# Kernel optimization log

Measured on AMD Instinct MI355X. Metric: run time of the kernel, lower is better.

Reference implementation:

```python
import jax, jax.numpy as jnp
import numpy as np
from jax import lax

DIM, DH, HEADS, IMG, P = 3, 32, 8, 64, 16
INNER = DH * HEADS            # 256
PATCH_DIM = DIM * P * P       # 768
HP = IMG // P                 # 4
EPS = 1e-5


def _conv3(x, w):
    # 3x3, stride 1, pad 1, no bias (NCHW / OIHW)
    return lax.conv_general_dilated(x, w, (1, 1), ((1, 1), (1, 1)),
                                    dimension_numbers=('NCHW', 'OIHW', 'NCHW'))


def _ln(x, g, b):
    mu = jnp.mean(x, axis=-1, keepdims=True)
    var = jnp.mean(jnp.square(x - mu), axis=-1, keepdims=True)
    return (x - mu) * lax.rsqrt(var + EPS) * g + b


def _attn(q, k, v):
    # q,k,v: [b, h, n, d]
    scores = jnp.einsum('bhnd,bhmd->bhnm', q, k) / np.float32(np.sqrt(DH))
    w = jax.nn.softmax(scores, axis=-1)
    return jnp.einsum('bhnm,bhmd->bhnd', w, v)


def _split_heads(qkv, b, n):
    # qkv: [b, n, 3*INNER] -> three [b, heads, n, dh]
    q, k, v = jnp.split(qkv, 3, axis=-1)
    f = lambda t: t.reshape(b, n, HEADS, DH).transpose(0, 2, 1, 3)
    return f(q), f(k), f(v)


def setup_inputs() -> dict:
    key = jax.random.key(0)
    ks = jax.random.split(key, 16)
    s = 0.02
    inp = {
        'x': jax.random.normal(ks[0], (1, DIM, IMG, IMG), jnp.float32),
        'pe_w1': jax.random.normal(ks[1], (DIM, DIM, 3, 3), jnp.float32) * s,
        'pe_w2': jax.random.normal(ks[2], (DIM, DIM, 3, 3), jnp.float32) * s,
        'embed_w': jax.random.normal(ks[3], (PATCH_DIM, DIM, P, P), jnp.float32) * s,
        'embed_b': jnp.zeros((PATCH_DIM,), jnp.float32),
        'ln1_g': jnp.ones((PATCH_DIM,), jnp.float32),
        'ln1_b': jnp.zeros((PATCH_DIM,), jnp.float32),
        'qkv_patch_w': jax.random.normal(ks[4], (PATCH_DIM, 3 * INNER), jnp.float32) * s,
        'proj_patch_w': jax.random.normal(ks[5], (INNER, PATCH_DIM), jnp.float32) * s,
        'proj_patch_b': jnp.zeros((PATCH_DIM,), jnp.float32),
        'recon_w': jax.random.normal(ks[6], (PATCH_DIM, DIM, P, P), jnp.float32) * s,
        'recon_b': jnp.zeros((DIM,), jnp.float32),
        'ln2_g': jnp.ones((DIM,), jnp.float32),
        'ln2_b': jnp.zeros((DIM,), jnp.float32),
        'qkv_seq_w': jax.random.normal(ks[7], (DIM, 3 * INNER), jnp.float32) * s,
        'proj_seq_w': jax.random.normal(ks[8], (INNER, DIM), jnp.float32) * s,
        'proj_seq_b': jnp.zeros((DIM,), jnp.float32),
        'pd_w1': jax.random.normal(ks[9], (DIM, DIM, 3, 3), jnp.float32) * s,
        'pd_w2': jax.random.normal(ks[10], (DIM, DIM, 3, 3), jnp.float32) * s,
    }
    return inp


def reference(x, pe_w1, pe_w2, embed_w, embed_b, ln1_g, ln1_b, qkv_patch_w,
              proj_patch_w, proj_patch_b, recon_w, recon_b, ln2_g, ln2_b,
              qkv_seq_w, proj_seq_w, proj_seq_b, pd_w1, pd_w2):
    b, c, h, w = x.shape
    pos = _conv3(jax.nn.gelu(_conv3(x, pe_w1), approximate=False), pe_w2)

    # ---- patch branch: strided conv == patch einsum ----
    xp = pos.reshape(b, c, HP, P, HP, P)
    patches = jnp.einsum('bchpwq,ocpq->bohw', xp, embed_w) + embed_b[None, :, None, None]
    patches = patches.reshape(b, PATCH_DIM, HP * HP).transpose(0, 2, 1)  # [b, 16, 768]
    pn = _ln(patches, ln1_g, ln1_b)
    q, k, v = _split_heads(pn @ qkv_patch_w, b, HP * HP)
    op = _attn(q, k, v)                                       # [b, heads, 16, dh]
    op = op.transpose(0, 2, 1, 3).reshape(b, HP * HP, INNER)
    op = op @ proj_patch_w + proj_patch_b                     # [b, 16, 768]
    op = op.transpose(0, 2, 1).reshape(b, PATCH_DIM, HP, HP)
    # ConvTranspose2d with k = stride = P -> einsum + reshape
    out_patch = jnp.einsum('bchw,cdij->bdhiwj', op, recon_w).reshape(b, DIM, h, w)
    out_patch = out_patch + recon_b[None, :, None, None]

    # ---- pixel-level branch: full dense attention over N = h*w tokens ----
    seq = pos.reshape(b, c, h * w).transpose(0, 2, 1)          # [b, N, 3]
    sn = _ln(seq, ln2_g, ln2_b)
    qs, ks_, vs = _split_heads(sn @ qkv_seq_w, b, h * w)
    os_ = _attn(qs, ks_, vs)                                   # [b, heads, N, dh]
    os_ = os_.transpose(0, 2, 1, 3).reshape(b, h * w, INNER)
    os_ = os_ @ proj_seq_w + proj_seq_b                         # [b, N, 3]
    out_seq = os_.transpose(0, 2, 1).reshape(b, DIM, h, w)

    combined = out_patch + out_seq
    return _conv3(jax.nn.gelu(_conv3(combined, pd_w1), approximate=False), pd_w2)
```

## Files before the change

### kernel.cpp

```cpp
#include <hip/hip_runtime.h>
#include <math.h>

#define NPIX 4096

__device__ __forceinline__ float gelu_exact(float x) {
    return 0.5f * x * (1.0f + erff(x * 0.70710678118654752440f));
}

__device__ __forceinline__ float conv3_tap(const float* __restrict__ src,
                                           const float* __restrict__ w,
                                           int o, int y, int x) {
    float acc = 0.f;
#pragma unroll
    for (int ci = 0; ci < 3; ++ci) {
#pragma unroll
        for (int dy = 0; dy < 3; ++dy) {
            int yy = y + dy - 1;
            if (yy < 0 || yy >= 64) continue;
#pragma unroll
            for (int dx = 0; dx < 3; ++dx) {
                int xx = x + dx - 1;
                if (xx < 0 || xx >= 64) continue;
                acc = fmaf(src[ci*NPIX + yy*64 + xx], w[o*27 + ci*9 + dy*3 + dx], acc);
            }
        }
    }
    return acc;
}

__global__ void kA(const float* __restrict__ x, const float* __restrict__ pew1,
                   const float* __restrict__ qsw, const float* __restrict__ psw,
                   float* __restrict__ t1, float* __restrict__ MT) {
    int b = blockIdx.x, tid = threadIdx.x;
    if (b < 48) {
        int idx = b*256 + tid;
        int c = idx >> 12, rem = idx & 4095;
        t1[idx] = gelu_exact(conv3_tap(x, pew1, c, rem >> 6, rem & 63));
    } else if (tid < 144) {
        int isT = tid >= 72;
        int u = isT ? tid - 72 : tid;
        int h = u / 9, i = (u % 9) / 3, j = u % 3;
        float acc = 0.f;
        if (!isT) {
            const float* wq = qsw + i*768 + h*32;
            const float* wk = qsw + j*768 + 256 + h*32;
#pragma unroll
            for (int d = 0; d < 32; ++d) acc = fmaf(wq[d], wk[d], acc);
            acc *= 1.4426950408889634f * 0.17677669529663687f;
        } else {
            const float* wv = qsw + i*768 + 512 + h*32;
#pragma unroll
            for (int d = 0; d < 32; ++d) acc = fmaf(wv[d], psw[(h*32 + d)*3 + j], acc);
        }
        MT[tid] = acc;
    }
}

__global__ void kB(const float* __restrict__ t1, const float* __restrict__ pew2,
                   const float* __restrict__ lg, const float* __restrict__ lb,
                   float* __restrict__ pos, float* __restrict__ sn,
                   float* __restrict__ z1, float* __restrict__ z2,
                   float* __restrict__ z3, float* __restrict__ z4) {
    int n = blockIdx.x*256 + threadIdx.x;
    int y = n >> 6, x = n & 63;
    float p0 = conv3_tap(t1, pew2, 0, y, x);
    float p1 = conv3_tap(t1, pew2, 1, y, x);
    float p2 = conv3_tap(t1, pew2, 2, y, x);
    float mu = (p0 + p1 + p2) * (1.f/3.f);
    float d0 = p0 - mu, d1 = p1 - mu, d2 = p2 - mu;
    float r = rsqrtf((d0*d0 + d1*d1 + d2*d2) * (1.f/3.f) + 1e-5f);
    pos[n] = p0; pos[NPIX+n] = p1; pos[2*NPIX+n] = p2;
    sn[n]        = d0*r*lg[0] + lb[0];
    sn[NPIX+n]   = d1*r*lg[1] + lb[1];
    sn[2*NPIX+n] = d2*r*lg[2] + lb[2];
#pragma unroll
    for (int i = 0; i < 3; ++i) {
        z1[i*NPIX+n] = 0.f; z2[i*NPIX+n] = 0.f;
        z3[i*NPIX+n] = 0.f; z4[i*NPIX+n] = 0.f;
    }
}

__global__ void kC1(const float* __restrict__ pos, const float* __restrict__ ew,
                    float* __restrict__ pb) {
    __shared__ float pv[16*96];
    int och = blockIdx.x % 3, ks = blockIdx.x / 3;
    int k0 = ks * 96, tid = threadIdx.x;
    for (int idx = tid; idx < 1536; idx += 256) {
        int t = idx / 96, k = idx % 96;
        int kk = k0 + k;
        int c = kk >> 8, p = (kk >> 4) & 15, q = kk & 15;
        int hp = t >> 2, wp = t & 3;
        pv[idx] = pos[c*NPIX + (hp*16 + p)*64 + wp*16 + q];
    }
    __syncthreads();
    int o = och*256 + tid;
    float acc[16];
#pragma unroll
    for (int t = 0; t < 16; ++t) acc[t] = 0.f;
    const float4* wr = (const float4*)(ew + o*768 + k0);
#pragma unroll 2
    for (int k4 = 0; k4 < 24; ++k4) {
        float4 w4 = wr[k4];
#pragma unroll
        for (int t = 0; t < 16; ++t) {
            const float* p4 = &pv[t*96 + k4*4];
            acc[t] = fmaf(w4.x, p4[0], acc[t]);
            acc[t] = fmaf(w4.y, p4[1], acc[t]);
            acc[t] = fmaf(w4.z, p4[2], acc[t]);
            acc[t] = fmaf(w4.w, p4[3], acc[t]);
        }
    }
#pragma unroll
    for (int t = 0; t < 16; ++t) atomicAdd(&pb[t*768 + o], acc[t]);
}

__global__ void kC2(const float* __restrict__ pb, const float* __restrict__ eb,
                    const float* __restrict__ g, const float* __restrict__ bb,
                    float* __restrict__ pn) {
    __shared__ float rs[12], rs2[12], stats[2];
    int t = blockIdx.x, tid = threadIdx.x;
    float v = pb[t*768 + tid] + eb[tid];
    float s = v, s2 = v*v;
#pragma unroll
    for (int o = 32; o >= 1; o >>= 1) { s += __shfl_xor(s, o); s2 += __shfl_xor(s2, o); }
    int wid = tid >> 6;
    if ((tid & 63) == 0) { rs[wid] = s; rs2[wid] = s2; }
    __syncthreads();
    if (tid == 0) {
        float S = 0.f, S2 = 0.f;
        for (int i = 0; i < 12; ++i) { S += rs[i]; S2 += rs2[i]; }
        float mu = S * (1.f/768.f);
        stats[0] = mu;
        stats[1] = rsqrtf(fmaxf(S2 * (1.f/768.f) - mu*mu, 0.f) + 1e-5f);
    }
    __syncthreads();
    pn[t*768 + tid] = (v - stats[0]) * stats[1] * g[tid] + bb[tid];
}

__global__ void kD(const float* __restrict__ pn, const float* __restrict__ qw,
                   float* __restrict__ qkvp) {
    __shared__ float ps[16*48];
    int och = blockIdx.x % 3, ks = blockIdx.x / 3;
    int k0 = ks * 48, tid = threadIdx.x;
    for (int idx = tid; idx < 768; idx += 256) {
        int t = idx / 48, k = idx % 48;
        ps[idx] = pn[t*768 + k0 + k];
    }
    __syncthreads();
    int o = och*256 + tid;
    float acc[16];
#pragma unroll
    for (int t = 0; t < 16; ++t) acc[t] = 0.f;
    for (int k = 0; k < 48; ++k) {
        float w = qw[(k0 + k)*768 + o];
#pragma unroll
        for (int t = 0; t < 16; ++t) acc[t] = fmaf(ps[t*48 + k], w, acc[t]);
    }
#pragma unroll
    for (int t = 0; t < 16; ++t) atomicAdd(&qkvp[t*768 + o], acc[t]);
}

__global__ __launch_bounds__(512) void kE(const float* __restrict__ qkvp,
                                          float* __restrict__ attn) {
    __shared__ float qs[16*772];
    __shared__ float wsm[8][16][16];
    int tid = threadIdx.x;
    for (int i = tid; i < 3072; i += 512) {
        int n = i / 192, c4 = i % 192;
        ((float4*)&qs[n*772])[c4] = ((const float4*)qkvp)[i];
    }
    __syncthreads();
    int h = tid >> 6, l = tid & 63;
    int nn = l >> 2, mg = l & 3;
    const float* q = &qs[nn*772 + h*32];
    float sc[4];
#pragma unroll
    for (int mm = 0; mm < 4; ++mm) {
        int m = mg*4 + mm;
        const float* k = &qs[m*772 + 256 + h*32];
        float d = 0.f;
#pragma unroll
        for (int dd = 0; dd < 32; ++dd) d = fmaf(q[dd], k[dd], d);
        sc[mm] = d * 0.17677669529663687f;
    }
    float mx = fmaxf(fmaxf(sc[0], sc[1]), fmaxf(sc[2], sc[3]));
    mx = fmaxf(mx, __shfl_xor(mx, 1));
    mx = fmaxf(mx, __shfl_xor(mx, 2));
    float e[4]; float sum = 0.f;
#pragma unroll
    for (int mm = 0; mm < 4; ++mm) { e[mm] = expf(sc[mm] - mx); sum += e[mm]; }
    sum += __shfl_xor(sum, 1);
    sum += __shfl_xor(sum, 2);
    float inv = 1.f / sum;
#pragma unroll
    for (int mm = 0; mm < 4; ++mm) wsm[h][nn][mg*4 + mm] = e[mm] * inv;
    __syncthreads();
    int flat = tid * 8;
    int h2 = flat >> 9, n2 = (flat >> 5) & 15, d0 = flat & 31;
    float out[8];
#pragma unroll
    for (int r = 0; r < 8; ++r) out[r] = 0.f;
#pragma unroll
    for (int m = 0; m < 16; ++m) {
        float ww = wsm[h2][n2][m];
        const float* v = &qs[m*772 + 512 + h2*32 + d0];
#pragma unroll
        for (int r = 0; r < 8; ++r) out[r] = fmaf(ww, v[r], out[r]);
    }
#pragma unroll
    for (int r = 0; r < 8; ++r) attn[n2*256 + h2*32 + d0 + r] = out[r];
}

__global__ void kF1(const float* __restrict__ at, const float* __restrict__ pw,
                    float* __restrict__ op) {
    __shared__ float as_[16*64];
    int och = blockIdx.x % 3, ks = blockIdx.x / 3;
    int k0 = ks * 64, tid = threadIdx.x;
    for (int idx = tid; idx < 1024; idx += 256) {
        int t = idx >> 6, k = idx & 63;
        as_[idx] = at[t*256 + k0 + k];
    }
    __syncthreads();
    int o = och*256 + tid;
    float acc[16];
#pragma unroll
    for (int t = 0; t < 16; ++t) acc[t] = 0.f;
    for (int k = 0; k < 64; ++k) {
        float w = pw[(k0 + k)*768 + o];
#pragma unroll
        for (int t = 0; t < 16; ++t) acc[t] = fmaf(as_[t*64 + k], w, acc[t]);
    }
#pragma unroll
    for (int t = 0; t < 16; ++t) atomicAdd(&op[t*768 + o], acc[t]);
}

__global__ void kF2(const float* __restrict__ op, const float* __restrict__ ppb,
                    const float* __restrict__ rw, float* __restrict__ outp) {
    __shared__ float os_[16*96];
    int dch = blockIdx.x % 3, cs = blockIdx.x / 3;
    int c0 = cs * 96, tid = threadIdx.x;
    for (int idx = tid; idx < 1536; idx += 256) {
        int t = idx / 96, k = idx % 96;
        os_[idx] = op[t*768 + c0 + k] + ppb[c0 + k];
    }
    __syncthreads();
    int dij = dch*256 + tid;
    float acc[16];
#pragma unroll
    for (int t = 0; t < 16; ++t) acc[t] = 0.f;
    for (int k = 0; k < 96; ++k) {
        float w = rw[(c0 + k)*768 + dij];
#pragma unroll
        for (int t = 0; t < 16; ++t) acc[t] = fmaf(os_[t*96 + k], w, acc[t]);
    }
    int d = dij >> 8, i = (dij >> 4) & 15, j = dij & 15;
#pragma unroll
    for (int t = 0; t < 16; ++t) {
        int hp = t >> 2, wp = t & 3;
        atomicAdd(&outp[d*NPIX + (hp*16 + i)*64 + wp*16 + j], acc[t]);
    }
}

__global__ __launch_bounds__(256) void kG(const float* __restrict__ snG,
                                          const float* __restrict__ MT,
                                          const float* __restrict__ psb,
                                          float* __restrict__ outs) {
    __shared__ float s[12288];
    __shared__ float Msh[72], Tsh[72];
    __shared__ float acc[8][3];
    int tid = threadIdx.x;
    for (int i = tid; i < 3072; i += 256)
        ((float4*)s)[i] = ((const float4*)snG)[i];
    if (tid < 72) Msh[tid] = MT[tid];
    else if (tid < 144) Tsh[tid - 72] = MT[tid];
    if (tid < 24) acc[tid / 3][tid % 3] = 0.f;
    __syncthreads();

    int pair = tid >> 2, chunk = tid & 3;
    int h = pair & 7, nl = pair >> 3;
    int n = blockIdx.x*8 + nl;
    float x0 = s[n], x1 = s[4096 + n], x2 = s[8192 + n];
    const float* M = &Msh[h*9];
    float a0 = x0*M[0] + x1*M[3] + x2*M[6];
    float a1 = x0*M[1] + x1*M[4] + x2*M[7];
    float a2 = x0*M[2] + x1*M[5] + x2*M[8];
    float Z = 0.f, S0 = 0.f, S1 = 0.f, S2 = 0.f;
#pragma unroll 4
    for (int t4 = 0; t4 < 1024; ++t4) {
        int m = t4*4 + chunk;
        float v0 = s[m], v1 = s[4096 + m], v2 = s[8192 + m];
        float e = exp2f(fmaf(a0, v0, fmaf(a1, v1, a2 * v2)));
        Z += e;
        S0 = fmaf(e, v0, S0); S1 = fmaf(e, v1, S1); S2 = fmaf(e, v2, S2);
    }
#pragma unroll
    for (int o = 1; o <= 2; o <<= 1) {
        Z  += __shfl_xor(Z, o);  S0 += __shfl_xor(S0, o);
        S1 += __shfl_xor(S1, o); S2 += __shfl_xor(S2, o);
    }
    if (chunk == 0) {
        float inv = 1.f / Z;
        float r0 = S0*inv, r1 = S1*inv, r2 = S2*inv;
        const float* T = &Tsh[h*9];
        atomicAdd(&acc[nl][0], r0*T[0] + r1*T[3] + r2*T[6]);
        atomicAdd(&acc[nl][1], r0*T[1] + r1*T[4] + r2*T[7]);
        atomicAdd(&acc[nl][2], r0*T[2] + r1*T[5] + r2*T[8]);
    }
    __syncthreads();
    if (tid < 24) {
        int j = tid % 3, nn = tid / 3;
        outs[j*NPIX + blockIdx.x*8 + nn] = acc[nn][j] + psb[j];
    }
}

__global__ void kH(const float* __restrict__ outp, const float* __restrict__ outs,
                   const float* __restrict__ rb, const float* __restrict__ w,
                   float* __restrict__ t2) {
    int idx = blockIdx.x*256 + threadIdx.x;
    int c = idx >> 12, rem = idx & 4095;
    int y = rem >> 6, x = rem & 63;
    float acc = 0.f;
#pragma unroll
    for (int ci = 0; ci < 3; ++ci) {
        float bias = rb[ci];
#pragma unroll
        for (int dy = 0; dy < 3; ++dy) {
            int yy = y + dy - 1;
            if (yy < 0 || yy >= 64) continue;
#pragma unroll
            for (int dx = 0; dx < 3; ++dx) {
                int xx = x + dx - 1;
                if (xx < 0 || xx >= 64) continue;
                float cb = outp[ci*NPIX + yy*64 + xx] + bias + outs[ci*NPIX + yy*64 + xx];
                acc = fmaf(cb, w[c*27 + ci*9 + dy*3 + dx], acc);
            }
        }
    }
    t2[idx] = gelu_exact(acc);
}

__global__ void kI(const float* __restrict__ t2, const float* __restrict__ w,
                   float* __restrict__ out) {
    int idx = blockIdx.x*256 + threadIdx.x;
    int c = idx >> 12, rem = idx & 4095;
    out[idx] = conv3_tap(t2, w, c, rem >> 6, rem & 63);
}

extern "C" void kernel_launch(void* const* d_in, const int* in_sizes, int n_in,
                              void* d_out, int out_size, void* d_ws, size_t ws_size,
                              hipStream_t stream) {
    (void)in_sizes; (void)n_in; (void)out_size; (void)ws_size;
    const float* x    = (const float*)d_in[0];
    const float* pew1 = (const float*)d_in[1];
    const float* pew2 = (const float*)d_in[2];
    const float* ew   = (const float*)d_in[3];
    const float* eb   = (const float*)d_in[4];
    const float* g1   = (const float*)d_in[5];
    const float* b1   = (const float*)d_in[6];
    const float* qpw  = (const float*)d_in[7];
    const float* ppw  = (const float*)d_in[8];
    const float* ppb  = (const float*)d_in[9];
    const float* rw   = (const float*)d_in[10];
    const float* rb   = (const float*)d_in[11];
    const float* g2   = (const float*)d_in[12];
    const float* b2   = (const float*)d_in[13];
    const float* qsw  = (const float*)d_in[14];
    const float* psw  = (const float*)d_in[15];
    const float* psb  = (const float*)d_in[16];
    const float* pdw1 = (const float*)d_in[17];
    const float* pdw2 = (const float*)d_in[18];

    float* ws   = (float*)d_ws;
    float* t1   = ws;
    float* pos  = ws + 12288;
    float* sn   = ws + 24576;
    float* MT   = ws + 36864;
    float* pb   = ws + 37008;
    float* pn   = ws + 49296;
    float* qkvp = ws + 61584;
    float* attn = ws + 73872;
    float* op   = ws + 77968;
    float* outp = ws + 90256;
    float* outs = ws + 102544;
    float* t2   = ws + 114832;
    float* out  = (float*)d_out;

    kA<<<dim3(49),  dim3(256), 0, stream>>>(x, pew1, qsw, psw, t1, MT);
    kB<<<dim3(16),  dim3(256), 0, stream>>>(t1, pew2, g2, b2, pos, sn, pb, qkvp, op, outp);
    kC1<<<dim3(24), dim3(256), 0, stream>>>(pos, ew, pb);
    kC2<<<dim3(16), dim3(768), 0, stream>>>(pb, eb, g1, b1, pn);
    kD<<<dim3(48),  dim3(256), 0, stream>>>(pn, qpw, qkvp);
    kE<<<dim3(1),   dim3(512), 0, stream>>>(qkvp, attn);
    kF1<<<dim3(12), dim3(256), 0, stream>>>(attn, ppw, op);
    kF2<<<dim3(24), dim3(256), 0, stream>>>(op, ppb, rw, outp);
    kG<<<dim3(512), dim3(256), 0, stream>>>(sn, MT, psb, outs);
    kH<<<dim3(48),  dim3(256), 0, stream>>>(outp, outs, rb, pdw1, t2);
    kI<<<dim3(48),  dim3(256), 0, stream>>>(t2, pdw2, out);
}
```

Measured before the change: 244.3 us.

## Fuse conv stages, merge pixel attention with embed GEMM, restructure patch attention

Merges the first two 3x3 convs into one kernel with a halo-recomputed intermediate in shared memory, and does the same for the final two convs. The pixel-attention kernel is rewritten so each thread handles one key subset for all eight heads using a hardware exp2. That kernel also shares a launch with the patch-embedding GEMM, which now uses a finer K split. Patch attention is folded into the output-projection kernel, and the kD and kF2 K-splits are doubled. The aim is to cut launch count, global round-trips and serial tail kernels, at the cost of redundant halo recomputation and more atomics.

```diff
diff --git a/kernel.cpp b/kernel.cpp
--- a/kernel.cpp
+++ b/kernel.cpp
@@ -2,6 +2,12 @@
 #include <math.h>
 
 #define NPIX 4096
+
+#if __has_builtin(__builtin_amdgcn_exp2f)
+#define EXP2(x) __builtin_amdgcn_exp2f(x)
+#else
+#define EXP2(x) exp2f(x)
+#endif
 
 __device__ __forceinline__ float gelu_exact(float x) {
     return 0.5f * x * (1.0f + erff(x * 0.70710678118654752440f));
@@ -28,90 +34,199 @@
     return acc;
 }
 
-__global__ void kA(const float* __restrict__ x, const float* __restrict__ pew1,
-                   const float* __restrict__ qsw, const float* __restrict__ psw,
-                   float* __restrict__ t1, float* __restrict__ MT) {
+__global__ __launch_bounds__(256) void kAB(
+        const float* __restrict__ x, const float* __restrict__ pew1,
+        const float* __restrict__ pew2,
+        const float* __restrict__ lg, const float* __restrict__ lb,
+        const float* __restrict__ qsw, const float* __restrict__ psw,
+        float* __restrict__ pos, float* __restrict__ sn, float* __restrict__ MT,
+        float* __restrict__ z1, float* __restrict__ z2,
+        float* __restrict__ z3, float* __restrict__ z4) {
     int b = blockIdx.x, tid = threadIdx.x;
-    if (b < 48) {
-        int idx = b*256 + tid;
-        int c = idx >> 12, rem = idx & 4095;
-        t1[idx] = gelu_exact(conv3_tap(x, pew1, c, rem >> 6, rem & 63));
-    } else if (tid < 144) {
-        int isT = tid >= 72;
-        int u = isT ? tid - 72 : tid;
-        int h = u / 9, i = (u % 9) / 3, j = u % 3;
+    if (b == 16) {
+        if (tid < 144) {
+            int isT = tid >= 72;
+            int u = isT ? tid - 72 : tid;
+            int h = u / 9, i = (u % 9) / 3, j = u % 3;
+            float acc = 0.f;
+            if (!isT) {
+                const float* wq = qsw + i*768 + h*32;
+                const float* wk = qsw + j*768 + 256 + h*32;
+#pragma unroll
+                for (int d = 0; d < 32; ++d) acc = fmaf(wq[d], wk[d], acc);
+                acc *= 1.4426950408889634f * 0.17677669529663687f;
+            } else {
+                const float* wv = qsw + i*768 + 512 + h*32;
+#pragma unroll
+                for (int d = 0; d < 32; ++d) acc = fmaf(wv[d], psw[(h*32 + d)*3 + j], acc);
+            }
+            MT[tid] = acc;
+        }
+        return;
+    }
+    __shared__ float t1l[3][8][64];
+    int y0 = b * 4;
+    for (int i = tid; i < 1536; i += 256) {
+        int c = i >> 9, rr = (i >> 6) & 7, xx = i & 63;
+        int yg = y0 - 2 + rr;
+        float v = 0.f;
+        if (yg >= 0 && yg < 64) v = gelu_exact(conv3_tap(x, pew1, c, yg, xx));
+        t1l[c][rr][xx] = v;
+    }
+    __syncthreads();
+    int n = b*256 + tid;
+    int yl = tid >> 6;
+    int xx = tid & 63;
+    int yg = y0 + yl;
+    float p[3];
+#pragma unroll
+    for (int o = 0; o < 3; ++o) {
         float acc = 0.f;
-        if (!isT) {
-            const float* wq = qsw + i*768 + h*32;
-            const float* wk = qsw + j*768 + 256 + h*32;
-#pragma unroll
-            for (int d = 0; d < 32; ++d) acc = fmaf(wq[d], wk[d], acc);
-            acc *= 1.4426950408889634f * 0.17677669529663687f;
-        } else {
-            const float* wv = qsw + i*768 + 512 + h*32;
-#pragma unroll
-            for (int d = 0; d < 32; ++d) acc = fmaf(wv[d], psw[(h*32 + d)*3 + j], acc);
-        }
-        MT[tid] = acc;
-    }
-}
-
-__global__ void kB(const float* __restrict__ t1, const float* __restrict__ pew2,
-                   const float* __restrict__ lg, const float* __restrict__ lb,
-                   float* __restrict__ pos, float* __restrict__ sn,
-                   float* __restrict__ z1, float* __restrict__ z2,
-                   float* __restrict__ z3, float* __restrict__ z4) {
-    int n = blockIdx.x*256 + threadIdx.x;
-    int y = n >> 6, x = n & 63;
-    float p0 = conv3_tap(t1, pew2, 0, y, x);
-    float p1 = conv3_tap(t1, pew2, 1, y, x);
-    float p2 = conv3_tap(t1, pew2, 2, y, x);
-    float mu = (p0 + p1 + p2) * (1.f/3.f);
-    float d0 = p0 - mu, d1 = p1 - mu, d2 = p2 - mu;
+#pragma unroll
+        for (int ci = 0; ci < 3; ++ci) {
+#pragma unroll
+            for (int dy = 0; dy < 3; ++dy) {
+                int yy = yg + dy - 1;
+                if (yy < 0 || yy >= 64) continue;
+                int rl = yl + dy + 1;
+#pragma unroll
+                for (int dx = 0; dx < 3; ++dx) {
+                    int xc = xx + dx - 1;
+                    if (xc < 0 || xc >= 64) continue;
+                    acc = fmaf(t1l[ci][rl][xc], pew2[o*27 + ci*9 + dy*3 + dx], acc);
+                }
+            }
+        }
+        p[o] = acc;
+    }
+    float mu = (p[0] + p[1] + p[2]) * (1.f/3.f);
+    float d0 = p[0]-mu, d1 = p[1]-mu, d2 = p[2]-mu;
     float r = rsqrtf((d0*d0 + d1*d1 + d2*d2) * (1.f/3.f) + 1e-5f);
-    pos[n] = p0; pos[NPIX+n] = p1; pos[2*NPIX+n] = p2;
+    pos[n] = p[0]; pos[NPIX+n] = p[1]; pos[2*NPIX+n] = p[2];
     sn[n]        = d0*r*lg[0] + lb[0];
     sn[NPIX+n]   = d1*r*lg[1] + lb[1];
     sn[2*NPIX+n] = d2*r*lg[2] + lb[2];
 #pragma unroll
-    for (int i = 0; i < 3; ++i) {
-        z1[i*NPIX+n] = 0.f; z2[i*NPIX+n] = 0.f;
-        z3[i*NPIX+n] = 0.f; z4[i*NPIX+n] = 0.f;
-    }
-}
-
-__global__ void kC1(const float* __restrict__ pos, const float* __restrict__ ew,
-                    float* __restrict__ pb) {
-    __shared__ float pv[16*96];
-    int och = blockIdx.x % 3, ks = blockIdx.x / 3;
-    int k0 = ks * 96, tid = threadIdx.x;
-    for (int idx = tid; idx < 1536; idx += 256) {
-        int t = idx / 96, k = idx % 96;
-        int kk = k0 + k;
-        int c = kk >> 8, p = (kk >> 4) & 15, q = kk & 15;
-        int hp = t >> 2, wp = t & 3;
-        pv[idx] = pos[c*NPIX + (hp*16 + p)*64 + wp*16 + q];
-    }
-    __syncthreads();
-    int o = och*256 + tid;
-    float acc[16];
-#pragma unroll
-    for (int t = 0; t < 16; ++t) acc[t] = 0.f;
-    const float4* wr = (const float4*)(ew + o*768 + k0);
-#pragma unroll 2
-    for (int k4 = 0; k4 < 24; ++k4) {
-        float4 w4 = wr[k4];
-#pragma unroll
-        for (int t = 0; t < 16; ++t) {
-            const float* p4 = &pv[t*96 + k4*4];
-            acc[t] = fmaf(w4.x, p4[0], acc[t]);
-            acc[t] = fmaf(w4.y, p4[1], acc[t]);
-            acc[t] = fmaf(w4.z, p4[2], acc[t]);
-            acc[t] = fmaf(w4.w, p4[3], acc[t]);
-        }
-    }
-#pragma unroll
-    for (int t = 0; t < 16; ++t) atomicAdd(&pb[t*768 + o], acc[t]);
+    for (int j = 0; j < 3; ++j) {
+        int idx = n*3 + j;
+        z1[idx] = 0.f; z2[idx] = 0.f; z3[idx] = 0.f; z4[idx] = 0.f;
+    }
+}
+
+__global__ __launch_bounds__(256) void K2(
+        const float* __restrict__ snG, const float* __restrict__ MT,
+        const float* __restrict__ psb, float* __restrict__ outs,
+        const float* __restrict__ pos, const float* __restrict__ ew,
+        float* __restrict__ pb) {
+    __shared__ __align__(16) float smem[12672];
+    __shared__ float Msh[72], Tsh[72];
+    int tid = threadIdx.x;
+    if (blockIdx.x < 512) {
+        for (int i4 = tid; i4 < 3072; i4 += 256) {
+            int ch = i4 >> 10, j = i4 & 1023;
+            int m = j * 4;
+            int c = m >> 7, rm = m & 127;
+            float4 v = ((const float4*)snG)[i4];
+            *(float4*)&smem[ch*4224 + c*132 + rm] = v;
+        }
+        if (tid < 72) Msh[tid] = MT[tid];
+        else if (tid < 144) Tsh[tid - 72] = MT[tid];
+        __syncthreads();
+
+        int nl = tid >> 5, c = tid & 31;
+        int n = blockIdx.x*8 + nl;
+        float x0 = smem[(n>>7)*132 + (n&127)];
+        float x1 = smem[4224 + (n>>7)*132 + (n&127)];
+        float x2 = smem[8448 + (n>>7)*132 + (n&127)];
+        float a0[8], a1[8], a2[8];
+#pragma unroll
+        for (int h = 0; h < 8; ++h) {
+            const float* M = &Msh[h*9];
+            a0[h] = x0*M[0] + x1*M[3] + x2*M[6];
+            a1[h] = x0*M[1] + x1*M[4] + x2*M[7];
+            a2[h] = x0*M[2] + x1*M[5] + x2*M[8];
+        }
+        float Z[8], S0[8], S1[8], S2[8];
+#pragma unroll
+        for (int h = 0; h < 8; ++h) { Z[h]=0.f; S0[h]=0.f; S1[h]=0.f; S2[h]=0.f; }
+        const float4* p0 = (const float4*)&smem[c*132];
+        const float4* p1 = (const float4*)&smem[4224 + c*132];
+        const float4* p2 = (const float4*)&smem[8448 + c*132];
+        for (int t = 0; t < 32; ++t) {
+            float4 v0 = p0[t], v1 = p1[t], v2 = p2[t];
+#pragma unroll
+            for (int mm = 0; mm < 4; ++mm) {
+                float w0 = (mm==0)?v0.x:(mm==1)?v0.y:(mm==2)?v0.z:v0.w;
+                float w1 = (mm==0)?v1.x:(mm==1)?v1.y:(mm==2)?v1.z:v1.w;
+                float w2 = (mm==0)?v2.x:(mm==1)?v2.y:(mm==2)?v2.z:v2.w;
+#pragma unroll
+                for (int h = 0; h < 8; ++h) {
+                    float e = EXP2(fmaf(a0[h], w0, fmaf(a1[h], w1, a2[h]*w2)));
+                    Z[h] += e;
+                    S0[h] = fmaf(e, w0, S0[h]);
+                    S1[h] = fmaf(e, w1, S1[h]);
+                    S2[h] = fmaf(e, w2, S2[h]);
+                }
+            }
+        }
+#pragma unroll
+        for (int h = 0; h < 8; ++h) {
+#pragma unroll
+            for (int o = 1; o <= 16; o <<= 1) {
+                Z[h]  += __shfl_xor(Z[h], o);
+                S0[h] += __shfl_xor(S0[h], o);
+                S1[h] += __shfl_xor(S1[h], o);
+                S2[h] += __shfl_xor(S2[h], o);
+            }
+        }
+        if (c == 0) {
+            float o0 = 0.f, o1 = 0.f, o2 = 0.f;
+#pragma unroll
+            for (int h = 0; h < 8; ++h) {
+                float inv = 1.f / Z[h];
+                float r0 = S0[h]*inv, r1 = S1[h]*inv, r2 = S2[h]*inv;
+                const float* T = &Tsh[h*9];
+                o0 += r0*T[0] + r1*T[3] + r2*T[6];
+                o1 += r0*T[1] + r1*T[4] + r2*T[7];
+                o2 += r0*T[2] + r1*T[5] + r2*T[8];
+            }
+            outs[n]        = o0 + psb[0];
+            outs[NPIX+n]   = o1 + psb[1];
+            outs[2*NPIX+n] = o2 + psb[2];
+        }
+    } else {
+        int bb = blockIdx.x - 512;
+        int och = bb % 3, ks = bb / 3;
+        int k0 = ks * 48;
+        float* pv = smem;
+        for (int idx = tid; idx < 768; idx += 256) {
+            int t = idx / 48, k = idx % 48;
+            int kk = k0 + k;
+            int cc = kk >> 8, pp = (kk >> 4) & 15, q = kk & 15;
+            int hp = t >> 2, wp = t & 3;
+            pv[idx] = pos[cc*NPIX + (hp*16 + pp)*64 + wp*16 + q];
+        }
+        __syncthreads();
+        int o = och*256 + tid;
+        float acc[16];
+#pragma unroll
+        for (int t = 0; t < 16; ++t) acc[t] = 0.f;
+        const float4* wr = (const float4*)(ew + o*768 + k0);
+#pragma unroll 3
+        for (int k4 = 0; k4 < 12; ++k4) {
+            float4 w4 = wr[k4];
+#pragma unroll
+            for (int t = 0; t < 16; ++t) {
+                const float* p4 = &pv[t*48 + k4*4];
+                acc[t] = fmaf(w4.x, p4[0], acc[t]);
+                acc[t] = fmaf(w4.y, p4[1], acc[t]);
+                acc[t] = fmaf(w4.z, p4[2], acc[t]);
+                acc[t] = fmaf(w4.w, p4[3], acc[t]);
+            }
+        }
+#pragma unroll
+        for (int t = 0; t < 16; ++t) atomicAdd(&pb[t*768 + o], acc[t]);
+    }
 }
 
 __global__ void kC2(const float* __restrict__ pb, const float* __restrict__ eb,
@@ -139,119 +254,110 @@
 
 __global__ void kD(const float* __restrict__ pn, const float* __restrict__ qw,
                    float* __restrict__ qkvp) {
-    __shared__ float ps[16*48];
+    __shared__ float ps[16*24];
     int och = blockIdx.x % 3, ks = blockIdx.x / 3;
-    int k0 = ks * 48, tid = threadIdx.x;
+    int k0 = ks * 24, tid = threadIdx.x;
+    for (int idx = tid; idx < 384; idx += 256) {
+        int t = idx / 24, k = idx % 24;
+        ps[idx] = pn[t*768 + k0 + k];
+    }
+    __syncthreads();
+    int o = och*256 + tid;
+    float acc[16];
+#pragma unroll
+    for (int t = 0; t < 16; ++t) acc[t] = 0.f;
+    for (int k = 0; k < 24; ++k) {
+        float w = qw[(k0 + k)*768 + o];
+#pragma unroll
+        for (int t = 0; t < 16; ++t) acc[t] = fmaf(ps[t*24 + k], w, acc[t]);
+    }
+#pragma unroll
+    for (int t = 0; t < 16; ++t) atomicAdd(&qkvp[t*768 + o], acc[t]);
+}
+
+__global__ __launch_bounds__(256) void kF1(const float* __restrict__ qkvp,
+                                           const float* __restrict__ pw,
+                                           float* __restrict__ op) {
+    __shared__ float qsl[16*64], ksl[16*64], vsl[16*64], scl[512], att[16*64];
+    int och = blockIdx.x % 3, ks = blockIdx.x / 3;
+    int tid = threadIdx.x;
+    for (int idx = tid; idx < 1024; idx += 256) {
+        int t = idx >> 6, j = idx & 63;
+        qsl[idx] = qkvp[t*768 + ks*64 + j];
+        ksl[idx] = qkvp[t*768 + 256 + ks*64 + j];
+        vsl[idx] = qkvp[t*768 + 512 + ks*64 + j];
+    }
+    __syncthreads();
+#pragma unroll
+    for (int r = 0; r < 2; ++r) {
+        int sidx = tid*2 + r;
+        int hh = sidx >> 8, nn = (sidx >> 4) & 15, m = sidx & 15;
+        float d = 0.f;
+        const float* q = &qsl[nn*64 + hh*32];
+        const float* k = &ksl[m*64 + hh*32];
+#pragma unroll
+        for (int dd = 0; dd < 32; ++dd) d = fmaf(q[dd], k[dd], d);
+        scl[sidx] = d * 0.17677669529663687f;
+    }
+    __syncthreads();
+    if (tid < 32) {
+        int hh = tid >> 4, nn = tid & 15;
+        float* row = &scl[hh*256 + nn*16];
+        float mx = row[0];
+#pragma unroll
+        for (int m = 1; m < 16; ++m) mx = fmaxf(mx, row[m]);
+        float s = 0.f;
+#pragma unroll
+        for (int m = 0; m < 16; ++m) { float e = expf(row[m] - mx); row[m] = e; s += e; }
+        float inv = 1.f / s;
+#pragma unroll
+        for (int m = 0; m < 16; ++m) row[m] *= inv;
+    }
+    __syncthreads();
+    {
+        int j = tid & 63, ng = tid >> 6;
+        int hh = j >> 5;
+#pragma unroll
+        for (int nn = ng*4; nn < ng*4 + 4; ++nn) {
+            float acc = 0.f;
+#pragma unroll
+            for (int m = 0; m < 16; ++m)
+                acc = fmaf(scl[hh*256 + nn*16 + m], vsl[m*64 + j], acc);
+            att[nn*64 + j] = acc;
+        }
+    }
+    __syncthreads();
+    int o = och*256 + tid;
+    float acc[16];
+#pragma unroll
+    for (int t = 0; t < 16; ++t) acc[t] = 0.f;
+    for (int k = 0; k < 64; ++k) {
+        float w = pw[(ks*64 + k)*768 + o];
+#pragma unroll
+        for (int t = 0; t < 16; ++t) acc[t] = fmaf(att[t*64 + k], w, acc[t]);
+    }
+#pragma unroll
+    for (int t = 0; t < 16; ++t) atomicAdd(&op[t*768 + o], acc[t]);
+}
+
+__global__ void kF2(const float* __restrict__ op, const float* __restrict__ ppb,
+                    const float* __restrict__ rw, float* __restrict__ outp) {
+    __shared__ float os_[16*48];
+    int dch = blockIdx.x % 3, cs = blockIdx.x / 3;
+    int c0 = cs * 48, tid = threadIdx.x;
     for (int idx = tid; idx < 768; idx += 256) {
         int t = idx / 48, k = idx % 48;
-        ps[idx] = pn[t*768 + k0 + k];
-    }
-    __syncthreads();
-    int o = och*256 + tid;
+        os_[idx] = op[t*768 + c0 + k] + ppb[c0 + k];
+    }
+    __syncthreads();
+    int dij = dch*256 + tid;
     float acc[16];
 #pragma unroll
     for (int t = 0; t < 16; ++t) acc[t] = 0.f;
     for (int k = 0; k < 48; ++k) {
-        float w = qw[(k0 + k)*768 + o];
-#pragma unroll
-        for (int t = 0; t < 16; ++t) acc[t] = fmaf(ps[t*48 + k], w, acc[t]);
-    }
-#pragma unroll
-    for (int t = 0; t < 16; ++t) atomicAdd(&qkvp[t*768 + o], acc[t]);
-}
-
-__global__ __launch_bounds__(512) void kE(const float* __restrict__ qkvp,
-                                          float* __restrict__ attn) {
-    __shared__ float qs[16*772];
-    __shared__ float wsm[8][16][16];
-    int tid = threadIdx.x;
-    for (int i = tid; i < 3072; i += 512) {
-        int n = i / 192, c4 = i % 192;
-        ((float4*)&qs[n*772])[c4] = ((const float4*)qkvp)[i];
-    }
-    __syncthreads();
-    int h = tid >> 6, l = tid & 63;
-    int nn = l >> 2, mg = l & 3;
-    const float* q = &qs[nn*772 + h*32];
-    float sc[4];
-#pragma unroll
-    for (int mm = 0; mm < 4; ++mm) {
-        int m = mg*4 + mm;
-        const float* k = &qs[m*772 + 256 + h*32];
-        float d = 0.f;
-#pragma unroll
-        for (int dd = 0; dd < 32; ++dd) d = fmaf(q[dd], k[dd], d);
-        sc[mm] = d * 0.17677669529663687f;
-    }
-    float mx = fmaxf(fmaxf(sc[0], sc[1]), fmaxf(sc[2], sc[3]));
-    mx = fmaxf(mx, __shfl_xor(mx, 1));
-    mx = fmaxf(mx, __shfl_xor(mx, 2));
-    float e[4]; float sum = 0.f;
-#pragma unroll
-    for (int mm = 0; mm < 4; ++mm) { e[mm] = expf(sc[mm] - mx); sum += e[mm]; }
-    sum += __shfl_xor(sum, 1);
-    sum += __shfl_xor(sum, 2);
-    float inv = 1.f / sum;
-#pragma unroll
-    for (int mm = 0; mm < 4; ++mm) wsm[h][nn][mg*4 + mm] = e[mm] * inv;
-    __syncthreads();
-    int flat = tid * 8;
-    int h2 = flat >> 9, n2 = (flat >> 5) & 15, d0 = flat & 31;
-    float out[8];
-#pragma unroll
-    for (int r = 0; r < 8; ++r) out[r] = 0.f;
-#pragma unroll
-    for (int m = 0; m < 16; ++m) {
-        float ww = wsm[h2][n2][m];
-        const float* v = &qs[m*772 + 512 + h2*32 + d0];
-#pragma unroll
-        for (int r = 0; r < 8; ++r) out[r] = fmaf(ww, v[r], out[r]);
-    }
-#pragma unroll
-    for (int r = 0; r < 8; ++r) attn[n2*256 + h2*32 + d0 + r] = out[r];
-}
-
-__global__ void kF1(const float* __restrict__ at, const float* __restrict__ pw,
-                    float* __restrict__ op) {
-    __shared__ float as_[16*64];
-    int och = blockIdx.x % 3, ks = blockIdx.x / 3;
-    int k0 = ks * 64, tid = threadIdx.x;
-    for (int idx = tid; idx < 1024; idx += 256) {
-        int t = idx >> 6, k = idx & 63;
-        as_[idx] = at[t*256 + k0 + k];
-    }
-    __syncthreads();
-    int o = och*256 + tid;
-    float acc[16];
-#pragma unroll
-    for (int t = 0; t < 16; ++t) acc[t] = 0.f;
-    for (int k = 0; k < 64; ++k) {
-        float w = pw[(k0 + k)*768 + o];
-#pragma unroll
-        for (int t = 0; t < 16; ++t) acc[t] = fmaf(as_[t*64 + k], w, acc[t]);
-    }
-#pragma unroll
-    for (int t = 0; t < 16; ++t) atomicAdd(&op[t*768 + o], acc[t]);
-}
-
-__global__ void kF2(const float* __restrict__ op, const float* __restrict__ ppb,
-                    const float* __restrict__ rw, float* __restrict__ outp) {
-    __shared__ float os_[16*96];
-    int dch = blockIdx.x % 3, cs = blockIdx.x / 3;
-    int c0 = cs * 96, tid = threadIdx.x;
-    for (int idx = tid; idx < 1536; idx += 256) {
-        int t = idx / 96, k = idx % 96;
-        os_[idx] = op[t*768 + c0 + k] + ppb[c0 + k];
-    }
-    __syncthreads();
-    int dij = dch*256 + tid;
-    float acc[16];
-#pragma unroll
-    for (int t = 0; t < 16; ++t) acc[t] = 0.f;
-    for (int k = 0; k < 96; ++k) {
         float w = rw[(c0 + k)*768 + dij];
 #pragma unroll
-        for (int t = 0; t < 16; ++t) acc[t] = fmaf(os_[t*96 + k], w, acc[t]);
+        for (int t = 0; t < 16; ++t) acc[t] = fmaf(os_[t*48 + k], w, acc[t]);
     }
     int d = dij >> 8, i = (dij >> 4) & 15, j = dij & 15;
 #pragma unroll
@@ -261,89 +367,63 @@
     }
 }
 
-__global__ __launch_bounds__(256) void kG(const float* __restrict__ snG,
-                                          const float* __restrict__ MT,
-                                          const float* __restrict__ psb,
-                                          float* __restrict__ outs) {
-    __shared__ float s[12288];
-    __shared__ float Msh[72], Tsh[72];
-    __shared__ float acc[8][3];
-    int tid = threadIdx.x;
-    for (int i = tid; i < 3072; i += 256)
-        ((float4*)s)[i] = ((const float4*)snG)[i];
-    if (tid < 72) Msh[tid] = MT[tid];
-    else if (tid < 144) Tsh[tid - 72] = MT[tid];
-    if (tid < 24) acc[tid / 3][tid % 3] = 0.f;
-    __syncthreads();
-
-    int pair = tid >> 2, chunk = tid & 3;
-    int h = pair & 7, nl = pair >> 3;
-    int n = blockIdx.x*8 + nl;
-    float x0 = s[n], x1 = s[4096 + n], x2 = s[8192 + n];
-    const float* M = &Msh[h*9];
-    float a0 = x0*M[0] + x1*M[3] + x2*M[6];
-    float a1 = x0*M[1] + x1*M[4] + x2*M[7];
-    float a2 = x0*M[2] + x1*M[5] + x2*M[8];
-    float Z = 0.f, S0 = 0.f, S1 = 0.f, S2 = 0.f;
-#pragma unroll 4
-    for (int t4 = 0; t4 < 1024; ++t4) {
-        int m = t4*4 + chunk;
-        float v0 = s[m], v1 = s[4096 + m], v2 = s[8192 + m];
-        float e = exp2f(fmaf(a0, v0, fmaf(a1, v1, a2 * v2)));
-        Z += e;
-        S0 = fmaf(e, v0, S0); S1 = fmaf(e, v1, S1); S2 = fmaf(e, v2, S2);
-    }
-#pragma unroll
-    for (int o = 1; o <= 2; o <<= 1) {
-        Z  += __shfl_xor(Z, o);  S0 += __shfl_xor(S0, o);
-        S1 += __shfl_xor(S1, o); S2 += __shfl_xor(S2, o);
-    }
-    if (chunk == 0) {
-        float inv = 1.f / Z;
-        float r0 = S0*inv, r1 = S1*inv, r2 = S2*inv;
-        const float* T = &Tsh[h*9];
-        atomicAdd(&acc[nl][0], r0*T[0] + r1*T[3] + r2*T[6]);
-        atomicAdd(&acc[nl][1], r0*T[1] + r1*T[4] + r2*T[7]);
-        atomicAdd(&acc[nl][2], r0*T[2] + r1*T[5] + r2*T[8]);
-    }
-    __syncthreads();
-    if (tid < 24) {
-        int j = tid % 3, nn = tid / 3;
-        outs[j*NPIX + blockIdx.x*8 + nn] = acc[nn][j] + psb[j];
-    }
-}
-
-__global__ void kH(const float* __restrict__ outp, const float* __restrict__ outs,
-                   const float* __restrict__ rb, const float* __restrict__ w,
-                   float* __restrict__ t2) {
-    int idx = blockIdx.x*256 + threadIdx.x;
-    int c = idx >> 12, rem = idx & 4095;
-    int y = rem >> 6, x = rem & 63;
-    float acc = 0.f;
-#pragma unroll
-    for (int ci = 0; ci < 3; ++ci) {
-        float bias = rb[ci];
-#pragma unroll
-        for (int dy = 0; dy < 3; ++dy) {
-            int yy = y + dy - 1;
-            if (yy < 0 || yy >= 64) continue;
-#pragma unroll
-            for (int dx = 0; dx < 3; ++dx) {
-                int xx = x + dx - 1;
-                if (xx < 0 || xx >= 64) continue;
-                float cb = outp[ci*NPIX + yy*64 + xx] + bias + outs[ci*NPIX + yy*64 + xx];
-                acc = fmaf(cb, w[c*27 + ci*9 + dy*3 + dx], acc);
-            }
-        }
-    }
-    t2[idx] = gelu_exact(acc);
-}
-
-__global__ void kI(const float* __restrict__ t2, const float* __restrict__ w,
-                   float* __restrict__ out) {
-    int idx = blockIdx.x*256 + threadIdx.x;
-    int c = idx >> 12, rem = idx & 4095;
-    out[idx] = conv3_tap(t2, w, c, rem >> 6, rem & 63);
+__global__ __launch_bounds__(256) void kHI(
+        const float* __restrict__ outp, const float* __restrict__ outs,
+        const float* __restrict__ rb, const float* __restrict__ w1,
+        const float* __restrict__ w2, float* __restrict__ out) {
+    __shared__ float t2l[3][8][64];
+    int b = blockIdx.x, tid = threadIdx.x;
+    int y0 = b * 4;
+    for (int i = tid; i < 1536; i += 256) {
+        int c = i >> 9, rr = (i >> 6) & 7, xx = i & 63;
+        int yg = y0 - 2 + rr;
+        float v = 0.f;
+        if (yg >= 0 && yg < 64) {
+            float acc = 0.f;
+#pragma unroll
+            for (int ci = 0; ci < 3; ++ci) {
+                float bias = rb[ci];
+#pragma unroll
+                for (int dy = 0; dy < 3; ++dy) {
+                    int yy = yg + dy - 1;
+                    if (yy < 0 || yy >= 64) continue;
+#pragma unroll
+                    for (int dx = 0; dx < 3; ++dx) {
+                        int xc = xx + dx - 1;
+                        if (xc < 0 || xc >= 64) continue;
+                        float cb = outp[ci*NPIX + yy*64 + xc] + bias
+                                 + outs[ci*NPIX + yy*64 + xc];
+                        acc = fmaf(cb, w1[c*27 + ci*9 + dy*3 + dx], acc);
+                    }
+                }
+            }
+            v = gelu_exact(acc);
+        }
+        t2l[c][rr][xx] = v;
+    }
+    __syncthreads();
+    int yl = tid >> 6, xx = tid & 63;
+    int yg = y0 + yl;
+#pragma unroll
+    for (int o = 0; o < 3; ++o) {
+        float acc = 0.f;
+#pragma unroll
+        for (int ci = 0; ci < 3; ++ci) {
+#pragma unroll
+            for (int dy = 0; dy < 3; ++dy) {
+                int yy = yg + dy - 1;
+                if (yy < 0 || yy >= 64) continue;
+                int rl = yl + dy + 1;
+#pragma unroll
+                for (int dx = 0; dx < 3; ++dx) {
+                    int xc = xx + dx - 1;
+                    if (xc < 0 || xc >= 64) continue;
+                    acc = fmaf(t2l[ci][rl][xc], w2[o*27 + ci*9 + dy*3 + dx], acc);
+                }
+            }
+        }
+        out[o*NPIX + yg*64 + xx] = acc;
+    }
 }
 
 extern "C" void kernel_launch(void* const* d_in, const int* in_sizes, int n_in,
@@ -371,29 +451,23 @@
     const float* pdw2 = (const float*)d_in[18];
 
     float* ws   = (float*)d_ws;
-    float* t1   = ws;
-    float* pos  = ws + 12288;
-    float* sn   = ws + 24576;
-    float* MT   = ws + 36864;
-    float* pb   = ws + 37008;
-    float* pn   = ws + 49296;
-    float* qkvp = ws + 61584;
-    float* attn = ws + 73872;
-    float* op   = ws + 77968;
-    float* outp = ws + 90256;
-    float* outs = ws + 102544;
-    float* t2   = ws + 114832;
+    float* pos  = ws;
+    float* sn   = ws + 12288;
+    float* MT   = ws + 24576;
+    float* pb   = ws + 24832;
+    float* pn   = ws + 37120;
+    float* qkvp = ws + 49408;
+    float* op   = ws + 61696;
+    float* outp = ws + 73984;
+    float* outs = ws + 86272;
     float* out  = (float*)d_out;
 
-    kA<<<dim3(49),  dim3(256), 0, stream>>>(x, pew1, qsw, psw, t1, MT);
-    kB<<<dim3(16),  dim3(256), 0, stream>>>(t1, pew2, g2, b2, pos, sn, pb, qkvp, op, outp);
-    kC1<<<dim3(24), dim3(256), 0, stream>>>(pos, ew, pb);
-    kC2<<<dim3(16), dim3(768), 0, stream>>>(pb, eb, g1, b1, pn);
-    kD<<<dim3(48),  dim3(256), 0, stream>>>(pn, qpw, qkvp);
-    kE<<<dim3(1),   dim3(512), 0, stream>>>(qkvp, attn);
-    kF1<<<dim3(12), dim3(256), 0, stream>>>(attn, ppw, op);
-    kF2<<<dim3(24), dim3(256), 0, stream>>>(op, ppb, rw, outp);
-    kG<<<dim3(512), dim3(256), 0, stream>>>(sn, MT, psb, outs);
-    kH<<<dim3(48),  dim3(256), 0, stream>>>(outp, outs, rb, pdw1, t2);
-    kI<<<dim3(48),  dim3(256), 0, stream>>>(t2, pdw2, out);
-}
+    kAB<<<dim3(17),  dim3(256), 0, stream>>>(x, pew1, pew2, g2, b2, qsw, psw,
+                                             pos, sn, MT, pb, qkvp, op, outp);
+    K2 <<<dim3(560), dim3(256), 0, stream>>>(sn, MT, psb, outs, pos, ew, pb);
+    kC2<<<dim3(16),  dim3(768), 0, stream>>>(pb, eb, g1, b1, pn);
+    kD <<<dim3(96),  dim3(256), 0, stream>>>(pn, qpw, qkvp);
+    kF1<<<dim3(12),  dim3(256), 0, stream>>>(qkvp, ppw, op);
+    kF2<<<dim3(48),  dim3(256), 0, stream>>>(op, ppb, rw, outp);
+    kHI<<<dim3(16),  dim3(256), 0, stream>>>(outp, outs, rb, pdw1, pdw2, out);
+}
```

Result: faster. 203.7 us (-16.6%).
